# Performance work log

Measured on AMD Instinct MI355X. Metric: run time of the kernel, lower is better.

## Reference

```python
import math
import jax, jax.numpy as jnp
import numpy as np

G = 96       # grid side; N = G*G tokens, one token per grid cell
D = 512      # d_model
R = 2        # radius (Chebyshev)
LN_EPS = 1e-5

# 24 neighbor offsets in the (2R+1)^2 window, excluding (0,0) (self is excluded in the torch code)
_OFF = np.array([(dx, dy) for dx in range(-R, R + 1) for dy in range(-R, R + 1) if not (dx == 0 and dy == 0)], dtype=np.int32)


def _layer_norm(x, g, b):
    m = jnp.mean(x, axis=-1, keepdims=True)
    v = jnp.mean(jnp.square(x - m), axis=-1, keepdims=True)
    return (x - m) * jax.lax.rsqrt(v + LN_EPS) * g + b


def setup_inputs() -> dict:
    key = jax.random.key(0)
    ks = jax.random.split(key, 12)
    N = G * G
    x = jax.random.normal(ks[0], (N, D), jnp.float32)
    gx, gy = jnp.meshgrid(jnp.arange(G), jnp.arange(G), indexing='ij')
    grid = jnp.stack([gx.ravel(), gy.ravel()], axis=-1).astype(jnp.int32)  # [N,2], one token per cell

    def lin(k, din, dout):
        return jax.random.normal(k, (din, dout), jnp.float32) * (1.0 / math.sqrt(din))

    return {
        'x': x, 'grid': grid,
        'Wq': lin(ks[1], D, D), 'bq': jnp.zeros((D,), jnp.float32),
        'Wk': lin(ks[2], D, D), 'bk': jnp.zeros((D,), jnp.float32),
        'Wv': lin(ks[3], D, D), 'bv': jnp.zeros((D,), jnp.float32),
        'Wo': lin(ks[4], D, D), 'bo': jnp.zeros((D,), jnp.float32),
        'g1': jnp.ones((D,), jnp.float32), 'b1': jnp.zeros((D,), jnp.float32),
        'g2': jnp.ones((D,), jnp.float32), 'b2': jnp.zeros((D,), jnp.float32),
        'W1': lin(ks[5], D, 4 * D), 'bf1': jnp.zeros((4 * D,), jnp.float32),
        'W2': lin(ks[6], 4 * D, D), 'bf2': jnp.zeros((D,), jnp.float32),
    }


def reference(x, grid, Wq, bq, Wk, bk, Wv, bv, Wo, bo, g1, b1, g2, b2, W1, bf1, W2, bf2):
    # dropout is identity (eval mode)
    h = _layer_norm(x, g1, b1)
    q = h @ Wq + bq
    k = h @ Wk + bk
    v = h @ Wv + bv

    off = jnp.asarray(_OFF)                      # [K=24, 2]
    nx = grid[:, 0:1] + off[None, :, 0]          # [N, K]
    ny = grid[:, 1:2] + off[None, :, 1]
    valid = (nx >= 0) & (nx < G) & (ny >= 0) & (ny < G)
    idx = jnp.where(valid, nx * G + ny, 0)       # row-major cell -> token index

    k_nbr = k[idx]                               # [N, K, D]
    v_nbr = v[idx]                               # [N, K, D]
    scores = jnp.einsum('nd,nkd->nk', q, k_nbr) / math.sqrt(D)
    neg = jnp.finfo(scores.dtype).min
    scores = jnp.where(valid, scores, neg)
    attn = jax.nn.softmax(scores, axis=-1)       # every token has >=8 valid neighbors for G>R
    out = jnp.einsum('nk,nkd->nd', attn, v_nbr)  # [N, D]

    x = x + out @ Wo + bo
    h2 = _layer_norm(x, g2, b2)
    ffn = jax.nn.gelu(h2 @ W1 + bf1, approximate=False) @ W2 + bf2
    return x + ffn
```

## Files before the change

### kernel.cpp

```cpp
#include <hip/hip_runtime.h>

typedef unsigned short u16;
typedef unsigned int u32;
typedef __bf16 bf16x8 __attribute__((ext_vector_type(8)));
typedef float f32x4 __attribute__((ext_vector_type(4)));

#define GRID_G 96
#define DMODEL 512
#define NTOK (GRID_G * GRID_G)

__device__ __forceinline__ u16 f2bf(float f) {
  return __builtin_bit_cast(u16, (__bf16)f);
}
__device__ __forceinline__ void unpack8(uint4 u, float* f) {
  f[0] = __builtin_bit_cast(float, u.x << 16);
  f[1] = __builtin_bit_cast(float, u.x & 0xffff0000u);
  f[2] = __builtin_bit_cast(float, u.y << 16);
  f[3] = __builtin_bit_cast(float, u.y & 0xffff0000u);
  f[4] = __builtin_bit_cast(float, u.z << 16);
  f[5] = __builtin_bit_cast(float, u.z & 0xffff0000u);
  f[6] = __builtin_bit_cast(float, u.w << 16);
  f[7] = __builtin_bit_cast(float, u.w & 0xffff0000u);
}
__device__ __forceinline__ float gelu_fast(float x) {
  float y = 0.7978845608f * (x + 0.044715f * x * x * x);
  float a = fabsf(y);
  float e = __expf(-2.0f * a);
  float th = (1.0f - e) / (1.0f + e);
  th = __builtin_copysignf(th, y);
  return 0.5f * x * (1.0f + th);
}

__device__ __forceinline__ void tr_tile(const float* __restrict__ src,
                                        u16* __restrict__ dst, int R, int C,
                                        int bx, int by, float (*tile)[33]) {
  int tx = threadIdx.x & 31, ty = threadIdx.x >> 5;
#pragma unroll
  for (int i = 0; i < 4; ++i) {
    int r = ty + i * 8;
    tile[r][tx] = src[(size_t)(by * 32 + r) * C + (bx * 32 + tx)];
  }
  __syncthreads();
#pragma unroll
  for (int i = 0; i < 4; ++i) {
    int c = ty + i * 8;
    dst[(size_t)(bx * 32 + c) * R + (by * 32 + tx)] = f2bf(tile[tx][c]);
  }
}

__global__ __launch_bounds__(256) void k_prep(
    const float* __restrict__ Wq, const float* __restrict__ Wk,
    const float* __restrict__ Wv, const float* __restrict__ Wo,
    const float* __restrict__ W1, const float* __restrict__ W2,
    const float* __restrict__ bq, const float* __restrict__ bk,
    const float* __restrict__ bv, const float* __restrict__ x,
    const float* __restrict__ g1, const float* __restrict__ b1,
    u16* __restrict__ WQT, u16* __restrict__ WKT, u16* __restrict__ WVT,
    u16* __restrict__ WOT, u16* __restrict__ W1T, u16* __restrict__ W2T,
    float* __restrict__ BCAT, u16* __restrict__ H) {
  __shared__ float tile[32][33];
  const int b = blockIdx.x;
  if (b < 1024) {
    int z = b >> 8, sub = b & 255;
    const float* s = z == 0 ? Wq : z == 1 ? Wk : z == 2 ? Wv : Wo;
    u16* d = z == 0 ? WQT : z == 1 ? WKT : z == 2 ? WVT : WOT;
    tr_tile(s, d, 512, 512, sub & 15, sub >> 4, tile);
  } else if (b < 2048) {
    int idx = b - 1024;
    tr_tile(W1, W1T, 512, 2048, idx & 63, idx >> 6, tile);
  } else if (b < 3072) {
    int idx = b - 2048;
    tr_tile(W2, W2T, 2048, 512, idx & 15, idx >> 4, tile);
  } else if (b < 3078) {
    int i = (b - 3072) * 256 + threadIdx.x;
    if (i < 512) BCAT[i] = bq[i];
    else if (i < 1024) BCAT[i] = bk[i - 512];
    else if (i < 1536) BCAT[i] = bv[i - 1024];
  } else {
    int tid = threadIdx.x, wid = tid >> 6, lane = tid & 63;
    int row = (b - 3078) * 4 + wid;
    const float* xr = x + (size_t)row * DMODEL;
    float4 v0 = *(const float4*)(xr + lane * 4);
    float4 v1 = *(const float4*)(xr + 256 + lane * 4);
    float s = v0.x + v0.y + v0.z + v0.w + v1.x + v1.y + v1.z + v1.w;
    float sq = v0.x * v0.x + v0.y * v0.y + v0.z * v0.z + v0.w * v0.w +
               v1.x * v1.x + v1.y * v1.y + v1.z * v1.z + v1.w * v1.w;
#pragma unroll
    for (int m = 1; m < 64; m <<= 1) {
      s += __shfl_xor(s, m);
      sq += __shfl_xor(sq, m);
    }
    float mean = s * (1.0f / DMODEL);
    float rstd = rsqrtf(sq * (1.0f / DMODEL) - mean * mean + 1e-5f);
    float4 ga = *(const float4*)(g1 + lane * 4);
    float4 gb = *(const float4*)(g1 + 256 + lane * 4);
    float4 ba = *(const float4*)(b1 + lane * 4);
    float4 bb = *(const float4*)(b1 + 256 + lane * 4);
    ushort4 o0, o1;
    o0.x = f2bf((v0.x - mean) * rstd * ga.x + ba.x);
    o0.y = f2bf((v0.y - mean) * rstd * ga.y + ba.y);
    o0.z = f2bf((v0.z - mean) * rstd * ga.z + ba.z);
    o0.w = f2bf((v0.w - mean) * rstd * ga.w + ba.w);
    o1.x = f2bf((v1.x - mean) * rstd * gb.x + bb.x);
    o1.y = f2bf((v1.y - mean) * rstd * gb.y + bb.y);
    o1.z = f2bf((v1.z - mean) * rstd * gb.z + bb.z);
    o1.w = f2bf((v1.w - mean) * rstd * gb.w + bb.w);
    u16* op = H + (size_t)row * DMODEL;
    *(ushort4*)(op + lane * 4) = o0;
    *(ushort4*)(op + 256 + lane * 4) = o1;
  }
}

__global__ __launch_bounds__(256) void k_layernorm_bf16(
    const float* __restrict__ x, const float* __restrict__ g,
    const float* __restrict__ b, u16* __restrict__ out) {
  int tid = threadIdx.x, wid = tid >> 6, lane = tid & 63;
  int row = blockIdx.x * 4 + wid;
  const float* xr = x + (size_t)row * DMODEL;
  float4 v0 = *(const float4*)(xr + lane * 4);
  float4 v1 = *(const float4*)(xr + 256 + lane * 4);
  float s = v0.x + v0.y + v0.z + v0.w + v1.x + v1.y + v1.z + v1.w;
  float sq = v0.x * v0.x + v0.y * v0.y + v0.z * v0.z + v0.w * v0.w +
             v1.x * v1.x + v1.y * v1.y + v1.z * v1.z + v1.w * v1.w;
#pragma unroll
  for (int m = 1; m < 64; m <<= 1) {
    s += __shfl_xor(s, m);
    sq += __shfl_xor(sq, m);
  }
  float mean = s * (1.0f / DMODEL);
  float rstd = rsqrtf(sq * (1.0f / DMODEL) - mean * mean + 1e-5f);
  float4 ga = *(const float4*)(g + lane * 4);
  float4 gb = *(const float4*)(g + 256 + lane * 4);
  float4 ba = *(const float4*)(b + lane * 4);
  float4 bb = *(const float4*)(b + 256 + lane * 4);
  ushort4 o0, o1;
  o0.x = f2bf((v0.x - mean) * rstd * ga.x + ba.x);
  o0.y = f2bf((v0.y - mean) * rstd * ga.y + ba.y);
  o0.z = f2bf((v0.z - mean) * rstd * ga.z + ba.z);
  o0.w = f2bf((v0.w - mean) * rstd * ga.w + ba.w);
  o1.x = f2bf((v1.x - mean) * rstd * gb.x + bb.x);
  o1.y = f2bf((v1.y - mean) * rstd * gb.y + bb.y);
  o1.z = f2bf((v1.z - mean) * rstd * gb.z + bb.z);
  o1.w = f2bf((v1.w - mean) * rstd * gb.w + bb.w);
  u16* op = out + (size_t)row * DMODEL;
  *(ushort4*)(op + lane * 4) = o0;
  *(ushort4*)(op + 256 + lane * 4) = o1;
}

__global__ __launch_bounds__(256) void k_attn(
    const u16* __restrict__ q, const u16* __restrict__ kk,
    const u16* __restrict__ vv, const int* __restrict__ gpos,
    u16* __restrict__ out) {
  int tid = threadIdx.x, wid = tid >> 6, lane = tid & 63;
  int n = blockIdx.x * 4 + wid;
  int px = gpos[2 * n], py = gpos[2 * n + 1];
  float qf[8];
  unpack8(*(const uint4*)(q + (size_t)n * DMODEL + lane * 8), qf);
  float sc[24];
  int nid[24];
  bool ok[24];
#pragma unroll
  for (int j = 0; j < 24; ++j) {
    int jj = j < 12 ? j : j + 1;
    int dx = jj / 5 - 2, dy = jj % 5 - 2;
    int nx = px + dx, ny = py + dy;
    bool val = (nx >= 0) && (nx < GRID_G) && (ny >= 0) && (ny < GRID_G);
    int id = val ? nx * GRID_G + ny : 0;
    ok[j] = val;
    nid[j] = id;
    float kf[8];
    unpack8(*(const uint4*)(kk + (size_t)id * DMODEL + lane * 8), kf);
    float p = 0.f;
#pragma unroll
    for (int e = 0; e < 8; ++e) p += qf[e] * kf[e];
#pragma unroll
    for (int m = 1; m < 64; m <<= 1) p += __shfl_xor(p, m);
    sc[j] = p * 0.04419417382415922f;
  }
  float mx = -3.0e38f;
#pragma unroll
  for (int j = 0; j < 24; ++j)
    if (ok[j]) mx = fmaxf(mx, sc[j]);
  float wsum = 0.f, w[24];
#pragma unroll
  for (int j = 0; j < 24; ++j) {
    w[j] = ok[j] ? expf(sc[j] - mx) : 0.f;
    wsum += w[j];
  }
  float inv = 1.0f / wsum;
  float acc[8] = {0, 0, 0, 0, 0, 0, 0, 0};
#pragma unroll
  for (int j = 0; j < 24; ++j) {
    float vf[8];
    unpack8(*(const uint4*)(vv + (size_t)nid[j] * DMODEL + lane * 8), vf);
    float wj = w[j];
#pragma unroll
    for (int e = 0; e < 8; ++e) acc[e] += wj * vf[e];
  }
  uint4 o;
  o.x = (u32)f2bf(acc[0] * inv) | ((u32)f2bf(acc[1] * inv) << 16);
  o.y = (u32)f2bf(acc[2] * inv) | ((u32)f2bf(acc[3] * inv) << 16);
  o.z = (u32)f2bf(acc[4] * inv) | ((u32)f2bf(acc[5] * inv) << 16);
  o.w = (u32)f2bf(acc[6] * inv) | ((u32)f2bf(acc[7] * inv) << 16);
  *(uint4*)(out + (size_t)n * DMODEL + lane * 8) = o;
}

#define BARR { __builtin_amdgcn_s_barrier(); __builtin_amdgcn_sched_barrier(0); }
#define WAIT8 asm volatile("s_waitcnt vmcnt(8)" ::: "memory");
#define WAIT0 asm volatile("s_waitcnt vmcnt(0)" ::: "memory");

template <int EPI>
__global__ __launch_bounds__(256, 2) void k_gemm(
    const u16* __restrict__ A, const u16* __restrict__ Bt,
    const float* __restrict__ bias, const float* __restrict__ res,
    float* __restrict__ outF, u16* __restrict__ outB,
    int M, int N, int K, int tiles_n) {
  __shared__ u16 lds[32768];
  const int t = threadIdx.x, wid = t >> 6, lane = t & 63;
  const int nwg = gridDim.x, bid = blockIdx.x;
  const int l = ((bid & 7) * (nwg >> 3)) + (bid >> 3);
  const int bM = (l / tiles_n) * 128, bN = (l % tiles_n) * 128;
  const int wr = wid >> 1, wc = wid & 1, lr = lane & 15, lg = lane >> 4;

  const int rs = lane >> 3;
  const int cl = (lane & 7) ^ rs;
  const u16* gA[4];
  const u16* gB[4];
  int dstL[4];
#pragma unroll
  for (int j = 0; j < 4; ++j) {
    int r = wid * 32 + j * 8 + rs;
    gA[j] = A + (size_t)(bM + r) * K + cl * 8;
    gB[j] = Bt + (size_t)(bN + r) * K + cl * 8;
    dstL[j] = wid * 2048 + j * 512;
  }

#define STAGE(BUF, KOFF)                                                              \
  {                                                                                   \
    _Pragma("unroll") for (int j = 0; j < 4; ++j) {                                   \
      __builtin_amdgcn_global_load_lds(                                               \
          (const __attribute__((address_space(1))) void*)(gA[j] + (KOFF)),            \
          (__attribute__((address_space(3))) void*)(lds + (BUF)*16384 + dstL[j]),     \
          16, 0, 0);                                                                  \
      __builtin_amdgcn_global_load_lds(                                               \
          (const __attribute__((address_space(1))) void*)(gB[j] + (KOFF)),            \
          (__attribute__((address_space(3))) void*)(lds + (BUF)*16384 + 8192 + dstL[j]), \
          16, 0, 0);                                                                  \
    }                                                                                 \
  }

  const int offA0 = (wr * 64 + lr) * 64 + ((0 + lg) ^ (lr & 7)) * 8;
  const int offA1 = (wr * 64 + lr) * 64 + ((4 + lg) ^ (lr & 7)) * 8;
  const int offB0 = (wc * 64 + lr) * 64 + ((0 + lg) ^ (lr & 7)) * 8;
  const int offB1 = (wc * 64 + lr) * 64 + ((4 + lg) ^ (lr & 7)) * 8;

  f32x4 acc[4][4];
#pragma unroll
  for (int i = 0; i < 4; ++i)
#pragma unroll
    for (int j = 0; j < 4; ++j) acc[i][j] = (f32x4){0.f, 0.f, 0.f, 0.f};

#define COMPUTE(BUF)                                                                  \
  {                                                                                   \
    _Pragma("unroll") for (int ks = 0; ks < 2; ++ks) {                                \
      const int oa = (BUF)*16384 + (ks ? offA1 : offA0);                              \
      const int ob = (BUF)*16384 + 8192 + (ks ? offB1 : offB0);                       \
      bf16x8 af[4], bfr[4];                                                           \
      _Pragma("unroll") for (int mt = 0; mt < 4; ++mt)                                \
          af[mt] = __builtin_bit_cast(bf16x8, *(const uint4*)(lds + oa + mt * 1024)); \
      _Pragma("unroll") for (int nt = 0; nt < 4; ++nt)                                \
          bfr[nt] = __builtin_bit_cast(bf16x8, *(const uint4*)(lds + ob + nt * 1024));\
      _Pragma("unroll") for (int mt = 0; mt < 4; ++mt)                                \
          _Pragma("unroll") for (int nt = 0; nt < 4; ++nt)                            \
              acc[mt][nt] = __builtin_amdgcn_mfma_f32_16x16x32_bf16(                  \
                  af[mt], bfr[nt], acc[mt][nt], 0, 0, 0);                             \
    }                                                                                 \
  }

  const int nk = K >> 6;
  STAGE(0, 0);
  int koff = 64;
  for (int tt = 0; tt < nk; tt += 2) {
    if (tt + 1 < nk) { STAGE(1, koff); WAIT8 } else { WAIT0 }
    BARR;
    COMPUTE(0);
    BARR;
    if (tt + 2 < nk) { STAGE(0, koff + 64); WAIT8 } else { WAIT0 }
    BARR;
    COMPUTE(1);
    BARR;
    koff += 128;
  }
#undef STAGE
#undef COMPUTE

#pragma unroll
  for (int mt = 0; mt < 4; ++mt) {
#pragma unroll
    for (int nt = 0; nt < 4; ++nt) {
      int col = bN + wc * 64 + nt * 16 + lr;
      float bc = bias[col];
      int row0 = bM + wr * 64 + mt * 16 + lg * 4;
#pragma unroll
      for (int r = 0; r < 4; ++r) {
        float val = acc[mt][nt][r] + bc;
        size_t off = (size_t)(row0 + r) * N + col;
        if constexpr (EPI == 1) {
          outF[off] = res[off] + val;
        } else {
          outB[off] = f2bf(val);
        }
      }
    }
  }
}

#define BARR2 { __builtin_amdgcn_sched_barrier(0); __builtin_amdgcn_s_barrier(); __builtin_amdgcn_sched_barrier(0); }
#define WAITV0 asm volatile("s_waitcnt vmcnt(0)" ::: "memory");
#define WAITV2 asm volatile("s_waitcnt vmcnt(2)" ::: "memory");
#define WAITV4 asm volatile("s_waitcnt vmcnt(4)" ::: "memory");

template <int EPI, int KDIM>
__global__ __launch_bounds__(512, 2) void k_gemm_big(
    const u16* __restrict__ A, const u16* __restrict__ Bt,
    const float* __restrict__ bias, u16* __restrict__ outB,
    int N, int tiles_n) {
  __shared__ u16 lds[65536];
  const int t = threadIdx.x, wid = t >> 6, lane = t & 63;
  const int wr = wid >> 2, wc = wid & 3;
  const int lr = lane & 15, lg = lane >> 4;
  const int nwg = gridDim.x, bid = blockIdx.x;
  const int qq = nwg >> 3, rr = nwg & 7;
  const int xcd = bid & 7, seq = bid >> 3;
  const int l = (xcd < rr ? xcd * (qq + 1) : rr * (qq + 1) + (xcd - rr) * qq) + seq;
  const int bM = (l / tiles_n) * 256, bN = (l % tiles_n) * 256;

  const int srow = wid * 8 + (lane >> 3);
  const int cl = (lane & 7) ^ (lane >> 3);
  const u16* pA = A + (size_t)(bM + srow) * KDIM + cl * 8;
  const u16* pB = Bt + (size_t)(bN + srow) * KDIM + cl * 8;
  const int dbase = wid * 512;

#define STG(C, BOFF, PTR, H, KT)                                                       \
  { _Pragma("unroll") for (int j = 0; j < 2; ++j)                                      \
      __builtin_amdgcn_global_load_lds(                                                \
        (const __attribute__((address_space(1))) void*)((PTR) + (size_t)((H)*128 + j*64) * KDIM + (KT)), \
        (__attribute__((address_space(3))) void*)(lds + (C) + (BOFF) + (H)*8192 + dbase + j*4096), \
        16, 0, 0); }

  const int swz0 = ((0 + lg) ^ (lr & 7)) * 8;
  const int swz1 = ((4 + lg) ^ (lr & 7)) * 8;

  f32x4 acc[4][8];
#pragma unroll
  for (int q = 0; q < 4; ++q)
#pragma unroll
    for (int rf = 0; rf < 8; ++rf) acc[q][rf] = (f32x4){0.f, 0.f, 0.f, 0.f};

  bf16x8 a[8][2], b0, b1;

#define READ_A(C)                                                                      \
  { _Pragma("unroll") for (int rf = 0; rf < 8; ++rf) {                                 \
      const u16* ab = lds + (C) + (wr * 128 + rf * 16 + lr) * 64;                      \
      a[rf][0] = __builtin_bit_cast(bf16x8, *(const uint4*)(ab + swz0));               \
      a[rf][1] = __builtin_bit_cast(bf16x8, *(const uint4*)(ab + swz1)); } }

#define READ_B(C, Q)                                                                   \
  { const u16* bb = lds + (C) + 16384 + ((Q)*64 + wc * 16 + lr) * 64;                  \
    b0 = __builtin_bit_cast(bf16x8, *(const uint4*)(bb + swz0));                       \
    b1 = __builtin_bit_cast(bf16x8, *(const uint4*)(bb + swz1)); }

#define MFMA_PH(Q)                                                                     \
  { __builtin_amdgcn_s_setprio(1);                                                     \
    _Pragma("unroll") for (int rf = 0; rf < 8; ++rf) {                                 \
      acc[Q][rf] = __builtin_amdgcn_mfma_f32_16x16x32_bf16(a[rf][0], b0, acc[Q][rf], 0, 0, 0); \
      acc[Q][rf] = __builtin_amdgcn_mfma_f32_16x16x32_bf16(a[rf][1], b1, acc[Q][rf], 0, 0, 0); } \
    __builtin_amdgcn_s_setprio(0); }

  STG(0, 0, pA, 0, 0); STG(0, 0, pA, 1, 0);
  STG(0, 16384, pB, 0, 0); STG(0, 16384, pB, 1, 0);
  WAITV0;
  BARR2;

  constexpr int nk = KDIM >> 6;
  for (int tt = 0; tt < nk; ++tt) {
    const int c = (tt & 1) << 15;
    const int cn = c ^ 32768;
    const int kn = (tt + 1) << 6;
    const bool pre = tt + 1 < nk;
    READ_A(c); READ_B(c, 0);
    if (pre) STG(cn, 0, pA, 0, kn);
    BARR2; MFMA_PH(0); BARR2;
    READ_B(c, 1);
    if (pre) { STG(cn, 0, pA, 1, kn); WAITV4 } else { WAITV0 }
    BARR2; MFMA_PH(1); BARR2;
    READ_B(c, 2);
    if (pre) STG(cn, 16384, pB, 0, kn);
    BARR2; MFMA_PH(2); BARR2;
    READ_B(c, 3);
    if (pre) { STG(cn, 16384, pB, 1, kn); WAITV2 }
    BARR2; MFMA_PH(3); BARR2;
  }
#undef STG
#undef READ_A
#undef READ_B
#undef MFMA_PH

#pragma unroll
  for (int q = 0; q < 4; ++q) {
    const int colb = bN + q * 64 + wc * 16 + lr;
    const float bc = bias[colb];
    if constexpr (EPI == 2) {
#pragma unroll
      for (int rf = 0; rf < 8; ++rf) {
        const int row0 = bM + wr * 128 + rf * 16 + lg * 4;
#pragma unroll
        for (int r = 0; r < 4; ++r)
          outB[(size_t)(row0 + r) * N + colb] = f2bf(gelu_fast(acc[q][rf][r] + bc));
      }
    } else {
      const int seg = colb >> 9;
      u16* base = outB + (size_t)seg * ((size_t)NTOK * DMODEL) + (colb & 511);
#pragma unroll
      for (int rf = 0; rf < 8; ++rf) {
        const int row0 = bM + wr * 128 + rf * 16 + lg * 4;
#pragma unroll
        for (int r = 0; r < 4; ++r)
          base[(size_t)(row0 + r) * DMODEL] = f2bf(acc[q][rf][r] + bc);
      }
    }
  }
}

extern "C" void kernel_launch(void* const* d_in, const int* in_sizes, int n_in,
                              void* d_out, int out_size, void* d_ws, size_t ws_size,
                              hipStream_t stream) {
  const float* x = (const float*)d_in[0];
  const int* gpos = (const int*)d_in[1];
  const float* Wq = (const float*)d_in[2];
  const float* bq = (const float*)d_in[3];
  const float* Wk = (const float*)d_in[4];
  const float* bk = (const float*)d_in[5];
  const float* Wv = (const float*)d_in[6];
  const float* bv = (const float*)d_in[7];
  const float* Wo = (const float*)d_in[8];
  const float* bo = (const float*)d_in[9];
  const float* g1 = (const float*)d_in[10];
  const float* b1 = (const float*)d_in[11];
  const float* g2 = (const float*)d_in[12];
  const float* b2 = (const float*)d_in[13];
  const float* W1 = (const float*)d_in[14];
  const float* bf1 = (const float*)d_in[15];
  const float* W2 = (const float*)d_in[16];
  const float* bf2 = (const float*)d_in[17];
  float* out = (float*)d_out;
  char* ws = (char*)d_ws;

  constexpr size_t SZ_W512 = (size_t)512 * 512 * 2;
  constexpr size_t SZ_W2048 = (size_t)512 * 2048 * 2;
  constexpr size_t SZ_ACT = (size_t)NTOK * 512 * 2;

  u16* WQT = (u16*)(ws + 0);
  u16* WKT = (u16*)(ws + SZ_W512);
  u16* WVT = (u16*)(ws + 2 * SZ_W512);
  u16* WOT = (u16*)(ws + 3 * SZ_W512);
  u16* W1T = (u16*)(ws + 4 * SZ_W512);
  u16* W2T = (u16*)(ws + 4 * SZ_W512 + SZ_W2048);
  float* BCAT = (float*)(ws + 4 * SZ_W512 + 2 * SZ_W2048);
  char* actbase = ws + 4 * SZ_W512 + 2 * SZ_W2048 + 6144;
  u16* H = (u16*)(actbase);
  u16* Q = (u16*)(actbase + SZ_ACT);
  u16* KB = (u16*)(actbase + 2 * SZ_ACT);
  u16* VB = (u16*)(actbase + 3 * SZ_ACT);
  u16* H2 = (u16*)(actbase + 4 * SZ_ACT);
  u16* U = (u16*)(actbase);

  k_prep<<<5382, 256, 0, stream>>>(Wq, Wk, Wv, Wo, W1, W2, bq, bk, bv, x, g1, b1,
                                   WQT, WKT, WVT, WOT, W1T, W2T, BCAT, H);

  k_gemm_big<3, 512><<<216, 512, 0, stream>>>(H, WQT, BCAT, Q, 1536, 6);

  k_attn<<<NTOK / 4, 256, 0, stream>>>(Q, KB, VB, gpos, H);

  k_gemm<1><<<288, 256, 0, stream>>>(H, WOT, bo, x, out, nullptr, NTOK, 512, 512, 4);

  k_layernorm_bf16<<<NTOK / 4, 256, 0, stream>>>(out, g2, b2, H2);

  k_gemm_big<2, 512><<<288, 512, 0, stream>>>(H2, W1T, bf1, U, 2048, 8);

  k_gemm<1><<<288, 256, 0, stream>>>(U, W2T, bf2, out, out, nullptr, NTOK, 512, 2048, 4);
}
```

Baseline: 170.8 us.

## Replace 256x256 big-tile GEMM with single-buffered 128x128 high-occupancy kernel

Swaps the 512-thread 256x256 double-buffered GEMM used for QKV and FFN-up with a new 256-thread 128x128 kernel. It uses a single 32KB LDS buffer and launch bounds of 4 blocks per CU. The aim is to raise occupancy and grid size (864 and 1152 blocks instead of 216 and 288), so waves on the CU hide load latency for each other instead of relying on in-kernel prefetch. In exchange, operand reuse per tile drops and the kernel waits for every K-step load with no overlap inside a block.

```diff
diff --git a/kernel.cpp b/kernel.cpp
--- a/kernel.cpp
+++ b/kernel.cpp
@@ -208,6 +208,7 @@
 #define BARR { __builtin_amdgcn_s_barrier(); __builtin_amdgcn_sched_barrier(0); }
 #define WAIT8 asm volatile("s_waitcnt vmcnt(8)" ::: "memory");
 #define WAIT0 asm volatile("s_waitcnt vmcnt(0)" ::: "memory");
+#define LGKM0 asm volatile("s_waitcnt lgkmcnt(0)" ::: "memory");
 
 template <int EPI>
 __global__ __launch_bounds__(256, 2) void k_gemm(
@@ -235,7 +236,7 @@
     dstL[j] = wid * 2048 + j * 512;
   }
 
-#define STAGE(BUF, KOFF)                                                              \
+#define STAGE1(BUF, KOFF)                                                             \
   {                                                                                   \
     _Pragma("unroll") for (int j = 0; j < 4; ++j) {                                   \
       __builtin_amdgcn_global_load_lds(                                               \
@@ -260,7 +261,7 @@
 #pragma unroll
     for (int j = 0; j < 4; ++j) acc[i][j] = (f32x4){0.f, 0.f, 0.f, 0.f};
 
-#define COMPUTE(BUF)                                                                  \
+#define COMPUTE1(BUF)                                                                 \
   {                                                                                   \
     _Pragma("unroll") for (int ks = 0; ks < 2; ++ks) {                                \
       const int oa = (BUF)*16384 + (ks ? offA1 : offA0);                              \
@@ -278,21 +279,21 @@
   }
 
   const int nk = K >> 6;
-  STAGE(0, 0);
+  STAGE1(0, 0);
   int koff = 64;
   for (int tt = 0; tt < nk; tt += 2) {
-    if (tt + 1 < nk) { STAGE(1, koff); WAIT8 } else { WAIT0 }
-    BARR;
-    COMPUTE(0);
-    BARR;
-    if (tt + 2 < nk) { STAGE(0, koff + 64); WAIT8 } else { WAIT0 }
-    BARR;
-    COMPUTE(1);
+    if (tt + 1 < nk) { STAGE1(1, koff); WAIT8 } else { WAIT0 }
+    BARR;
+    COMPUTE1(0);
+    BARR;
+    if (tt + 2 < nk) { STAGE1(0, koff + 64); WAIT8 } else { WAIT0 }
+    BARR;
+    COMPUTE1(1);
     BARR;
     koff += 128;
   }
-#undef STAGE
-#undef COMPUTE
+#undef STAGE1
+#undef COMPUTE1
 
 #pragma unroll
   for (int mt = 0; mt < 4; ++mt) {
@@ -315,118 +316,95 @@
   }
 }
 
-#define BARR2 { __builtin_amdgcn_sched_barrier(0); __builtin_amdgcn_s_barrier(); __builtin_amdgcn_sched_barrier(0); }
-#define WAITV0 asm volatile("s_waitcnt vmcnt(0)" ::: "memory");
-#define WAITV2 asm volatile("s_waitcnt vmcnt(2)" ::: "memory");
-#define WAITV4 asm volatile("s_waitcnt vmcnt(4)" ::: "memory");
-
-template <int EPI, int KDIM>
-__global__ __launch_bounds__(512, 2) void k_gemm_big(
+template <int EPI>
+__global__ __launch_bounds__(256, 4) void k_gemm_hi(
     const u16* __restrict__ A, const u16* __restrict__ Bt,
     const float* __restrict__ bias, u16* __restrict__ outB,
-    int N, int tiles_n) {
-  __shared__ u16 lds[65536];
+    int M, int N, int K, int tiles_n) {
+  __shared__ u16 lds[16384];
   const int t = threadIdx.x, wid = t >> 6, lane = t & 63;
-  const int wr = wid >> 2, wc = wid & 3;
-  const int lr = lane & 15, lg = lane >> 4;
   const int nwg = gridDim.x, bid = blockIdx.x;
-  const int qq = nwg >> 3, rr = nwg & 7;
-  const int xcd = bid & 7, seq = bid >> 3;
-  const int l = (xcd < rr ? xcd * (qq + 1) : rr * (qq + 1) + (xcd - rr) * qq) + seq;
-  const int bM = (l / tiles_n) * 256, bN = (l % tiles_n) * 256;
-
-  const int srow = wid * 8 + (lane >> 3);
-  const int cl = (lane & 7) ^ (lane >> 3);
-  const u16* pA = A + (size_t)(bM + srow) * KDIM + cl * 8;
-  const u16* pB = Bt + (size_t)(bN + srow) * KDIM + cl * 8;
-  const int dbase = wid * 512;
-
-#define STG(C, BOFF, PTR, H, KT)                                                       \
-  { _Pragma("unroll") for (int j = 0; j < 2; ++j)                                      \
-      __builtin_amdgcn_global_load_lds(                                                \
-        (const __attribute__((address_space(1))) void*)((PTR) + (size_t)((H)*128 + j*64) * KDIM + (KT)), \
-        (__attribute__((address_space(3))) void*)(lds + (C) + (BOFF) + (H)*8192 + dbase + j*4096), \
-        16, 0, 0); }
-
-  const int swz0 = ((0 + lg) ^ (lr & 7)) * 8;
-  const int swz1 = ((4 + lg) ^ (lr & 7)) * 8;
-
-  f32x4 acc[4][8];
-#pragma unroll
-  for (int q = 0; q < 4; ++q)
-#pragma unroll
-    for (int rf = 0; rf < 8; ++rf) acc[q][rf] = (f32x4){0.f, 0.f, 0.f, 0.f};
-
-  bf16x8 a[8][2], b0, b1;
-
-#define READ_A(C)                                                                      \
-  { _Pragma("unroll") for (int rf = 0; rf < 8; ++rf) {                                 \
-      const u16* ab = lds + (C) + (wr * 128 + rf * 16 + lr) * 64;                      \
-      a[rf][0] = __builtin_bit_cast(bf16x8, *(const uint4*)(ab + swz0));               \
-      a[rf][1] = __builtin_bit_cast(bf16x8, *(const uint4*)(ab + swz1)); } }
-
-#define READ_B(C, Q)                                                                   \
-  { const u16* bb = lds + (C) + 16384 + ((Q)*64 + wc * 16 + lr) * 64;                  \
-    b0 = __builtin_bit_cast(bf16x8, *(const uint4*)(bb + swz0));                       \
-    b1 = __builtin_bit_cast(bf16x8, *(const uint4*)(bb + swz1)); }
-
-#define MFMA_PH(Q)                                                                     \
-  { __builtin_amdgcn_s_setprio(1);                                                     \
-    _Pragma("unroll") for (int rf = 0; rf < 8; ++rf) {                                 \
-      acc[Q][rf] = __builtin_amdgcn_mfma_f32_16x16x32_bf16(a[rf][0], b0, acc[Q][rf], 0, 0, 0); \
-      acc[Q][rf] = __builtin_amdgcn_mfma_f32_16x16x32_bf16(a[rf][1], b1, acc[Q][rf], 0, 0, 0); } \
-    __builtin_amdgcn_s_setprio(0); }
-
-  STG(0, 0, pA, 0, 0); STG(0, 0, pA, 1, 0);
-  STG(0, 16384, pB, 0, 0); STG(0, 16384, pB, 1, 0);
-  WAITV0;
-  BARR2;
-
-  constexpr int nk = KDIM >> 6;
+  const int l = ((bid & 7) * (nwg >> 3)) + (bid >> 3);
+  const int bM = (l / tiles_n) * 128, bN = (l % tiles_n) * 128;
+  const int wr = wid >> 1, wc = wid & 1, lr = lane & 15, lg = lane >> 4;
+
+  const int rs = lane >> 3;
+  const int cl = (lane & 7) ^ rs;
+  const u16* gA[4];
+  const u16* gB[4];
+  int dstL[4];
+#pragma unroll
+  for (int j = 0; j < 4; ++j) {
+    int r = wid * 32 + j * 8 + rs;
+    gA[j] = A + (size_t)(bM + r) * K + cl * 8;
+    gB[j] = Bt + (size_t)(bN + r) * K + cl * 8;
+    dstL[j] = wid * 2048 + j * 512;
+  }
+
+  const int offA0 = (wr * 64 + lr) * 64 + ((0 + lg) ^ (lr & 7)) * 8;
+  const int offA1 = (wr * 64 + lr) * 64 + ((4 + lg) ^ (lr & 7)) * 8;
+  const int offB0 = 8192 + (wc * 64 + lr) * 64 + ((0 + lg) ^ (lr & 7)) * 8;
+  const int offB1 = 8192 + (wc * 64 + lr) * 64 + ((4 + lg) ^ (lr & 7)) * 8;
+
+  f32x4 acc[4][4];
+#pragma unroll
+  for (int i = 0; i < 4; ++i)
+#pragma unroll
+    for (int j = 0; j < 4; ++j) acc[i][j] = (f32x4){0.f, 0.f, 0.f, 0.f};
+
+  const int nk = K >> 6;
   for (int tt = 0; tt < nk; ++tt) {
-    const int c = (tt & 1) << 15;
-    const int cn = c ^ 32768;
-    const int kn = (tt + 1) << 6;
-    const bool pre = tt + 1 < nk;
-    READ_A(c); READ_B(c, 0);
-    if (pre) STG(cn, 0, pA, 0, kn);
-    BARR2; MFMA_PH(0); BARR2;
-    READ_B(c, 1);
-    if (pre) { STG(cn, 0, pA, 1, kn); WAITV4 } else { WAITV0 }
-    BARR2; MFMA_PH(1); BARR2;
-    READ_B(c, 2);
-    if (pre) STG(cn, 16384, pB, 0, kn);
-    BARR2; MFMA_PH(2); BARR2;
-    READ_B(c, 3);
-    if (pre) { STG(cn, 16384, pB, 1, kn); WAITV2 }
-    BARR2; MFMA_PH(3); BARR2;
-  }
-#undef STG
-#undef READ_A
-#undef READ_B
-#undef MFMA_PH
-
-#pragma unroll
-  for (int q = 0; q < 4; ++q) {
-    const int colb = bN + q * 64 + wc * 16 + lr;
-    const float bc = bias[colb];
-    if constexpr (EPI == 2) {
-#pragma unroll
-      for (int rf = 0; rf < 8; ++rf) {
-        const int row0 = bM + wr * 128 + rf * 16 + lg * 4;
-#pragma unroll
-        for (int r = 0; r < 4; ++r)
-          outB[(size_t)(row0 + r) * N + colb] = f2bf(gelu_fast(acc[q][rf][r] + bc));
-      }
-    } else {
-      const int seg = colb >> 9;
-      u16* base = outB + (size_t)seg * ((size_t)NTOK * DMODEL) + (colb & 511);
-#pragma unroll
-      for (int rf = 0; rf < 8; ++rf) {
-        const int row0 = bM + wr * 128 + rf * 16 + lg * 4;
-#pragma unroll
-        for (int r = 0; r < 4; ++r)
-          base[(size_t)(row0 + r) * DMODEL] = f2bf(acc[q][rf][r] + bc);
+    const int koff = tt << 6;
+#pragma unroll
+    for (int j = 0; j < 4; ++j) {
+      __builtin_amdgcn_global_load_lds(
+          (const __attribute__((address_space(1))) void*)(gA[j] + koff),
+          (__attribute__((address_space(3))) void*)(lds + dstL[j]), 16, 0, 0);
+      __builtin_amdgcn_global_load_lds(
+          (const __attribute__((address_space(1))) void*)(gB[j] + koff),
+          (__attribute__((address_space(3))) void*)(lds + 8192 + dstL[j]), 16, 0, 0);
+    }
+    WAIT0;
+    BARR;
+#pragma unroll
+    for (int ks = 0; ks < 2; ++ks) {
+      const int oa = ks ? offA1 : offA0;
+      const int ob = ks ? offB1 : offB0;
+      bf16x8 af[4], bfr[4];
+#pragma unroll
+      for (int mt = 0; mt < 4; ++mt)
+        af[mt] = __builtin_bit_cast(bf16x8, *(const uint4*)(lds + oa + mt * 1024));
+#pragma unroll
+      for (int nt = 0; nt < 4; ++nt)
+        bfr[nt] = __builtin_bit_cast(bf16x8, *(const uint4*)(lds + ob + nt * 1024));
+#pragma unroll
+      for (int mt = 0; mt < 4; ++mt)
+#pragma unroll
+        for (int nt = 0; nt < 4; ++nt)
+          acc[mt][nt] = __builtin_amdgcn_mfma_f32_16x16x32_bf16(af[mt], bfr[nt], acc[mt][nt], 0, 0, 0);
+    }
+    LGKM0;
+    BARR;
+  }
+
+#pragma unroll
+  for (int mt = 0; mt < 4; ++mt) {
+#pragma unroll
+    for (int nt = 0; nt < 4; ++nt) {
+      int col = bN + wc * 64 + nt * 16 + lr;
+      float bc = bias[col];
+      int row0 = bM + wr * 64 + mt * 16 + lg * 4;
+#pragma unroll
+      for (int r = 0; r < 4; ++r) {
+        float val = acc[mt][nt][r] + bc;
+        if constexpr (EPI == 2) {
+          outB[(size_t)(row0 + r) * N + col] = f2bf(gelu_fast(val));
+        } else {
+          int seg = col >> 9;
+          size_t off = (size_t)seg * ((size_t)NTOK * DMODEL) +
+                       (size_t)(row0 + r) * DMODEL + (col & 511);
+          outB[off] = f2bf(val);
+        }
       }
     }
   }
@@ -478,7 +456,7 @@
   k_prep<<<5382, 256, 0, stream>>>(Wq, Wk, Wv, Wo, W1, W2, bq, bk, bv, x, g1, b1,
                                    WQT, WKT, WVT, WOT, W1T, W2T, BCAT, H);
 
-  k_gemm_big<3, 512><<<216, 512, 0, stream>>>(H, WQT, BCAT, Q, 1536, 6);
+  k_gemm_hi<3><<<864, 256, 0, stream>>>(H, WQT, BCAT, Q, NTOK, 1536, 512, 12);
 
   k_attn<<<NTOK / 4, 256, 0, stream>>>(Q, KB, VB, gpos, H);
 
@@ -486,7 +464,7 @@
 
   k_layernorm_bf16<<<NTOK / 4, 256, 0, stream>>>(out, g2, b2, H2);
 
-  k_gemm_big<2, 512><<<288, 512, 0, stream>>>(H2, W1T, bf1, U, 2048, 8);
+  k_gemm_hi<2><<<1152, 256, 0, stream>>>(H2, W1T, bf1, U, NTOK, 2048, 512, 16);
 
   k_gemm<1><<<288, 256, 0, stream>>>(U, W2T, bf2, out, out, nullptr, NTOK, 512, 2048, 4);
 }
```

New measurement: 158.9 us. -7.0%, faster.
